# Kernel optimization log

Measured on AMD Instinct MI355X. Metric: run time of the kernel, lower is better.

Reference implementation:

```python
import jax, jax.numpy as jnp
import numpy as np

MAX_IT = 10
LAMBDA_ROF = 4.0
SIGMA = 1.0 / (7.0 * 0.01)
TAU = 0.01
THETA = 0.5
M, N = 2048, 2048


def forward_grad(x):
    """x: [1,M,N] -> [2,M,N]; forward differences, zero at last col/row."""
    gh = jnp.pad(x[0, :, 1:] - x[0, :, :-1], ((0, 0), (0, 1)))  # horizontal
    gv = jnp.pad(x[0, 1:, :] - x[0, :-1, :], ((0, 1), (0, 0)))  # vertical
    return jnp.stack([gh, gv], axis=0)


def backward_div(y):
    """y: [2,M,N] -> [1,M,N]; adjoint backward-difference divergence."""
    yh, yv = y[0], y[1]
    d_h = jnp.concatenate([yh[:, :1], yh[:, 1:-1] - yh[:, :-2], -yh[:, -2:-1]], axis=1)
    d_v = jnp.concatenate([yv[:1, :], yv[1:-1, :] - yv[:-2, :], -yv[-2:-1, :]], axis=0)
    return (d_h + d_v)[None]  # [1,M,N]


def prox_linf_ball(p, r):
    # Torch original builds m1/m2 from p.data (no grad flow) -> stop_gradient.
    m1 = jnp.maximum(p - r, 0.0)
    m2 = jnp.maximum(-p - r, 0.0)
    return p - jax.lax.stop_gradient(m1 - m2)  # == clamp(p, -r, r) in value


def setup_inputs() -> dict:
    key = jax.random.key(0)
    k1, k2 = jax.random.split(key)
    img_obs = jax.random.uniform(k1, (1, M, N), dtype=jnp.float32)
    w1 = jnp.array([0.5], dtype=jnp.float32)  # nn.Parameter [1]
    w2 = jnp.array([0.4], dtype=jnp.float32)  # nn.Parameter [1]
    return {"img_obs": img_obs, "w1": w1, "w2": w2}


def reference(img_obs, w1, w2):
    x = img_obs
    x_tilde = img_obs
    y = forward_grad(x)  # [2,M,N]
    # w_term built from y.data in torch -> constant wrt autodiff
    w_term = jax.lax.stop_gradient(jnp.exp(-jnp.abs(y)))
    w = w1[0] + w2[0] * w_term  # [2,M,N]
    for _ in range(MAX_IT):
        # dual weighted update + L-inf prox
        y = y + SIGMA * w * forward_grad(x_tilde)
        y = prox_linf_ball(y, 1.0)
        # primal weighted update (ROF)
        x_old = x
        x = (x + TAU * backward_div(w * y) + LAMBDA_ROF * TAU * img_obs) / (1.0 + LAMBDA_ROF * TAU)
        # primal over-relaxation
        x_tilde = x + THETA * (x - x_old)
    return x_tilde
```

## Files before the change

kernel.cpp:

```cpp
#include <hip/hip_runtime.h>


namespace {
constexpr int M = 2048, N = 2048;
constexpr float SIGMA     = 1.0f / (7.0f * 0.01f);
constexpr float TAU       = 0.01f;
constexpr float TAUIS     = TAU * (7.0f * 0.01f);
constexpr float LT        = 4.0f * 0.01f;
constexpr float INV_DEN   = 1.0f / (1.0f + 4.0f * 0.01f);
constexpr int TW = 64, TH = 64;
constexpr int PC = 88;
constexpr int PR = 84;
constexpr int UPR = 22;
constexpr int PROC = 83;
constexpr int NU = PROC * UPR;
constexpr int NT = 1024;
constexpr int NPASS = 2;
}

typedef _Float16 h4 __attribute__((ext_vector_type(4)));

__device__ inline h4 h4splat(float v) {
    _Float16 s = (_Float16)v;
    return (h4){s, s, s, s};
}
__device__ inline int imax(int a, int b) { return a > b ? a : b; }

__global__ __launch_bounds__(NT, 4) void pd_fused(
    const float* __restrict__ img, float* __restrict__ out,
    const float* __restrict__ w1p, const float* __restrict__ w2p)
{
    __shared__ __align__(16) float    sXT[PR * PC];
    __shared__ __align__(16) _Float16 sQH[PR * PC];
    __shared__ __align__(16) _Float16 sQV[PR * PC];

    const int tid  = threadIdx.x;
    const int lane = tid & 63;
    const int c0 = blockIdx.x * TW, r0 = blockIdx.y * TH;
    const int gr0 = r0 - 10, gc0 = c0 - 12;
    const float w1 = w1p[0], w2 = w2p[0];

    int u_[NPASS], bF_[NPASS], gi_[NPASS], gjb_[NPASS], dth_[NPASS];
    #pragma unroll
    for (int p = 0; p < NPASS; ++p) {
        int u = tid + p * NT;
        int li = u / UPR, uj = u - li * UPR;
        int lc = uj * 4;
        u_[p] = u; bF_[p] = u * 4;
        gi_[p] = gr0 + li; gjb_[p] = gc0 + lc;
        int d = imax(imax(9 - li, li - 73), imax(8 - lc, lc - 75));
        d = imax(d, 0);
        if (u >= NU) d = 100;
        dth_[p] = d;
    }

    #pragma unroll
    for (int p = 0; p < NPASS; ++p) {
        int su = tid + p * NT;
        if (su < PR * UPR) {
            int li = su / UPR, uj = su - li * UPR;
            int gi = gr0 + li, gj = gc0 + uj * 4;
            float4 v = make_float4(0.f, 0.f, 0.f, 0.f);
            if ((unsigned)gi < (unsigned)M && (unsigned)gj <= (unsigned)(N - 4))
                v = *(const float4*)&img[(size_t)gi * N + gj];
            *(float4*)&sXT[su * 4] = v;
        }
    }
    __syncthreads();

    float xr[NPASS][4], xi[NPASS][4], xt[NPASS][4];
    h4 yh[NPASS], yv[NPASS], swh[NPASS], swv[NPASS], qH[NPASS], qV[NPASS];

    #pragma unroll
    for (int p = 0; p < NPASS; ++p) {
        int u = u_[p], bF = bF_[p];
        float4 c = make_float4(0.f, 0.f, 0.f, 0.f);
        if (u < NU) c = *(const float4*)&sXT[bF];
        float rr = __shfl_down(c.x, 1, 64);
        if (u < NU) {
            if (lane == 63) rr = sXT[bF + 4];
            float4 dn = *(const float4*)&sXT[bF + PC];
            float ca[4] = {c.x, c.y, c.z, c.w};
            float da[4] = {dn.x, dn.y, dn.z, dn.w};
            int gi = gi_[p];
            bool rok = (unsigned)gi < (unsigned)M;
            bool vok = rok && (gi < M - 1);
            #pragma unroll
            for (int l = 0; l < 4; ++l) {
                int gj = gjb_[p] + l;
                bool cok = (unsigned)gj < (unsigned)N;
                bool hok = rok && cok && (gj < N - 1);
                bool vk  = vok && cok;
                float nxt = (l < 3) ? ca[l + 1] : rr;
                float gh = hok ? nxt - ca[l] : 0.f;
                float gv = vk  ? da[l] - ca[l] : 0.f;
                float wh = fmaf(w2, __expf(-fabsf(gh)), w1);
                float wv = fmaf(w2, __expf(-fabsf(gv)), w1);
                float y0h = fminf(fmaxf(gh * fmaf(SIGMA, wh, 1.f), -1.f), 1.f);
                float y0v = fminf(fmaxf(gv * fmaf(SIGMA, wv, 1.f), -1.f), 1.f);
                float sh = hok ? SIGMA * wh : 0.f;
                float sv = vk  ? SIGMA * wv : 0.f;
                yh[p][l]  = (_Float16)y0h;  yv[p][l]  = (_Float16)y0v;
                swh[p][l] = (_Float16)sh;   swv[p][l] = (_Float16)sv;
                qH[p][l]  = (_Float16)(sh * y0h);
                qV[p][l]  = (_Float16)(sv * y0v);
                xr[p][l] = ca[l]; xi[p][l] = ca[l]; xt[p][l] = ca[l];
            }
            *(h4*)&sQH[bF] = qH[p]; *(h4*)&sQV[bF] = qV[p];
        }
    }
    __syncthreads();

    auto dual = [&](int rem) {
        #pragma unroll
        for (int p = 0; p < NPASS; ++p) {
            float rr = __shfl_down(xt[p][0], 1, 64);
            if (rem >= dth_[p]) {
                int bF = bF_[p];
                if (lane == 63) rr = sXT[bF + 4];
                float4 dn = *(const float4*)&sXT[bF + PC];
                float da[4] = {dn.x, dn.y, dn.z, dn.w};
                h4 ghh, gvh;
                #pragma unroll
                for (int l = 0; l < 4; ++l) {
                    float nxt = (l < 3) ? xt[p][l + 1] : rr;
                    ghh[l] = (_Float16)(nxt - xt[p][l]);
                    gvh[l] = (_Float16)(da[l] - xt[p][l]);
                }
                h4 nh = yh[p] + swh[p] * ghh;
                h4 nv = yv[p] + swv[p] * gvh;
                nh = __builtin_elementwise_min(__builtin_elementwise_max(nh, h4splat(-1.f)), h4splat(1.f));
                nv = __builtin_elementwise_min(__builtin_elementwise_max(nv, h4splat(-1.f)), h4splat(1.f));
                yh[p] = nh; yv[p] = nv;
                h4 qh = swh[p] * nh;
                h4 qv = swv[p] * nv;
                qH[p] = qh; qV[p] = qv;
                *(h4*)&sQH[bF] = qh; *(h4*)&sQV[bF] = qv;
            }
        }
    };

    auto primal = [&](int rem) {
        #pragma unroll
        for (int p = 0; p < NPASS; ++p) {
            if (rem >= dth_[p]) {
                int u = u_[p], bF = bF_[p];
                int bu = (u >= UPR) ? bF - PC : bF;
                h4 qvu = *(const h4*)&sQV[bu];
                _Float16 qhl = sQH[imax(bF - 1, 0)];
                h4 qsh;
                qsh[0] = qhl; qsh[1] = qH[p][0]; qsh[2] = qH[p][1]; qsh[3] = qH[p][2];
                h4 dvg = (qH[p] - qsh) + (qV[p] - qvu);
                float xtv[4];
                #pragma unroll
                for (int l = 0; l < 4; ++l) {
                    float dv = (float)dvg[l];
                    float xo = xr[p][l];
                    float xn = (fmaf(TAUIS, dv, xo) + LT * xi[p][l]) * INV_DEN;
                    xr[p][l] = xn;
                    float v = fmaf(0.5f, xn - xo, xn);
                    xt[p][l] = v; xtv[l] = v;
                }
                *(float4*)&sXT[bF] = make_float4(xtv[0], xtv[1], xtv[2], xtv[3]);
            }
        }
    };

    primal(9);
    __syncthreads();
    #pragma unroll 1
    for (int t = 1; t < 10; ++t) {
        int rem = 9 - t;
        dual(rem);
        __syncthreads();
        primal(rem);
        __syncthreads();
    }

    {
        int row = tid >> 4;
        int cu  = tid & 15;
        float4 v = *(const float4*)&sXT[(10 + row) * PC + 12 + 4 * cu];
        *(float4*)&out[(size_t)(r0 + row) * N + (c0 + 4 * cu)] = v;
    }
}

extern "C" void kernel_launch(void* const* d_in, const int* in_sizes, int n_in,
                              void* d_out, int out_size, void* d_ws, size_t ws_size,
                              hipStream_t stream)
{
    const float* img = (const float*)d_in[0];
    const float* w1  = (const float*)d_in[1];
    const float* w2  = (const float*)d_in[2];
    float* out = (float*)d_out;

    dim3 grid(N / TW, M / TH);
    pd_fused<<<grid, NT, 0, stream>>>(img, out, w1, w2);
}
```

Baseline: 120.2 us.

## Shrink tiles to 64x48 with 512 threads and trim shared/register state

Reduces the tile height to 48 rows and the block to 512 threads, with three work units per thread, and adds a ragged-edge guard on the output store. To cut register and LDS pressure, the full sQH array is replaced by a small array that holds only the last horizontal-flux element of each unit, qV is reloaded from LDS instead of kept in registers, and the observed image copy is stored as fp16. The goal is more resident blocks per CU. The cost is a larger halo overhead relative to the tile (68 rows loaded for 48 output rows), a partial last block row, and extra fp16 rounding in the fidelity term.

```diff
diff --git a/kernel.cpp b/kernel.cpp
--- a/kernel.cpp
+++ b/kernel.cpp
@@ -8,14 +8,15 @@
 constexpr float TAUIS     = TAU * (7.0f * 0.01f);
 constexpr float LT        = 4.0f * 0.01f;
 constexpr float INV_DEN   = 1.0f / (1.0f + 4.0f * 0.01f);
-constexpr int TW = 64, TH = 64;
+constexpr int TW = 64, TH = 48;
 constexpr int PC = 88;
-constexpr int PR = 84;
+constexpr int PR = 68;
 constexpr int UPR = 22;
-constexpr int PROC = 83;
+constexpr int PROC = 67;
 constexpr int NU = PROC * UPR;
-constexpr int NT = 1024;
-constexpr int NPASS = 2;
+constexpr int NT = 512;
+constexpr int NPASS = 3;
+constexpr int GY = (M + TH - 1) / TH;
 }
 
 typedef _Float16 h4 __attribute__((ext_vector_type(4)));
@@ -31,8 +32,8 @@
     const float* __restrict__ w1p, const float* __restrict__ w2p)
 {
     __shared__ __align__(16) float    sXT[PR * PC];
-    __shared__ __align__(16) _Float16 sQH[PR * PC];
     __shared__ __align__(16) _Float16 sQV[PR * PC];
+    __shared__ __align__(16) _Float16 sQH3[1536];
 
     const int tid  = threadIdx.x;
     const int lane = tid & 63;
@@ -40,15 +41,14 @@
     const int gr0 = r0 - 10, gc0 = c0 - 12;
     const float w1 = w1p[0], w2 = w2p[0];
 
-    int u_[NPASS], bF_[NPASS], gi_[NPASS], gjb_[NPASS], dth_[NPASS];
+    int bF_[NPASS], dth_[NPASS];
     #pragma unroll
     for (int p = 0; p < NPASS; ++p) {
         int u = tid + p * NT;
         int li = u / UPR, uj = u - li * UPR;
         int lc = uj * 4;
-        u_[p] = u; bF_[p] = u * 4;
-        gi_[p] = gr0 + li; gjb_[p] = gc0 + lc;
-        int d = imax(imax(9 - li, li - 73), imax(8 - lc, lc - 75));
+        bF_[p] = u * 4;
+        int d = imax(imax(9 - li, li - (TH + 9)), imax(8 - lc, lc - 75));
         d = imax(d, 0);
         if (u >= NU) d = 100;
         dth_[p] = d;
@@ -68,26 +68,28 @@
     }
     __syncthreads();
 
-    float xr[NPASS][4], xi[NPASS][4], xt[NPASS][4];
-    h4 yh[NPASS], yv[NPASS], swh[NPASS], swv[NPASS], qH[NPASS], qV[NPASS];
+    float xr[NPASS][4], xt[NPASS][4];
+    h4 xi[NPASS], yh[NPASS], yv[NPASS], swh[NPASS], swv[NPASS], qH[NPASS];
 
     #pragma unroll
     for (int p = 0; p < NPASS; ++p) {
-        int u = u_[p], bF = bF_[p];
+        int u = tid + p * NT, bF = bF_[p];
         float4 c = make_float4(0.f, 0.f, 0.f, 0.f);
         if (u < NU) c = *(const float4*)&sXT[bF];
         float rr = __shfl_down(c.x, 1, 64);
         if (u < NU) {
+            int li = u / UPR;
+            int gi = gr0 + li, gjb = gc0 + (u - li * UPR) * 4;
             if (lane == 63) rr = sXT[bF + 4];
             float4 dn = *(const float4*)&sXT[bF + PC];
             float ca[4] = {c.x, c.y, c.z, c.w};
             float da[4] = {dn.x, dn.y, dn.z, dn.w};
-            int gi = gi_[p];
             bool rok = (unsigned)gi < (unsigned)M;
             bool vok = rok && (gi < M - 1);
+            h4 qv;
             #pragma unroll
             for (int l = 0; l < 4; ++l) {
-                int gj = gjb_[p] + l;
+                int gj = gjb + l;
                 bool cok = (unsigned)gj < (unsigned)N;
                 bool hok = rok && cok && (gj < N - 1);
                 bool vk  = vok && cok;
@@ -103,10 +105,12 @@
                 yh[p][l]  = (_Float16)y0h;  yv[p][l]  = (_Float16)y0v;
                 swh[p][l] = (_Float16)sh;   swv[p][l] = (_Float16)sv;
                 qH[p][l]  = (_Float16)(sh * y0h);
-                qV[p][l]  = (_Float16)(sv * y0v);
-                xr[p][l] = ca[l]; xi[p][l] = ca[l]; xt[p][l] = ca[l];
+                qv[l]     = (_Float16)(sv * y0v);
+                xr[p][l] = ca[l]; xt[p][l] = ca[l];
+                xi[p][l] = (_Float16)ca[l];
             }
-            *(h4*)&sQH[bF] = qH[p]; *(h4*)&sQV[bF] = qV[p];
+            *(h4*)&sQV[bF] = qv;
+            sQH3[u] = qH[p][3];
         }
     }
     __syncthreads();
@@ -134,8 +138,9 @@
                 yh[p] = nh; yv[p] = nv;
                 h4 qh = swh[p] * nh;
                 h4 qv = swv[p] * nv;
-                qH[p] = qh; qV[p] = qv;
-                *(h4*)&sQH[bF] = qh; *(h4*)&sQV[bF] = qv;
+                qH[p] = qh;
+                *(h4*)&sQV[bF] = qv;
+                sQH3[bF >> 2] = qh[3];
             }
         }
     };
@@ -144,19 +149,20 @@
         #pragma unroll
         for (int p = 0; p < NPASS; ++p) {
             if (rem >= dth_[p]) {
-                int u = u_[p], bF = bF_[p];
-                int bu = (u >= UPR) ? bF - PC : bF;
+                int bF = bF_[p];
+                int bu = (bF >= UPR * 4) ? bF - PC : bF;
                 h4 qvu = *(const h4*)&sQV[bu];
-                _Float16 qhl = sQH[imax(bF - 1, 0)];
+                h4 qv  = *(const h4*)&sQV[bF];
+                _Float16 qhl = sQH3[imax((bF >> 2) - 1, 0)];
                 h4 qsh;
                 qsh[0] = qhl; qsh[1] = qH[p][0]; qsh[2] = qH[p][1]; qsh[3] = qH[p][2];
-                h4 dvg = (qH[p] - qsh) + (qV[p] - qvu);
+                h4 dvg = (qH[p] - qsh) + (qv - qvu);
                 float xtv[4];
                 #pragma unroll
                 for (int l = 0; l < 4; ++l) {
                     float dv = (float)dvg[l];
                     float xo = xr[p][l];
-                    float xn = (fmaf(TAUIS, dv, xo) + LT * xi[p][l]) * INV_DEN;
+                    float xn = (fmaf(TAUIS, dv, xo) + LT * (float)xi[p][l]) * INV_DEN;
                     xr[p][l] = xn;
                     float v = fmaf(0.5f, xn - xo, xn);
                     xt[p][l] = v; xtv[l] = v;
@@ -177,11 +183,15 @@
         __syncthreads();
     }
 
-    {
-        int row = tid >> 4;
-        int cu  = tid & 15;
-        float4 v = *(const float4*)&sXT[(10 + row) * PC + 12 + 4 * cu];
-        *(float4*)&out[(size_t)(r0 + row) * N + (c0 + 4 * cu)] = v;
+    #pragma unroll
+    for (int v = tid; v < TH * (TW / 4); v += NT) {
+        int row = v >> 4;
+        int cu  = v & 15;
+        int gi = r0 + row;
+        if (gi < M) {
+            float4 o = *(const float4*)&sXT[(10 + row) * PC + 12 + 4 * cu];
+            *(float4*)&out[(size_t)gi * N + (c0 + 4 * cu)] = o;
+        }
     }
 }
 
@@ -194,6 +204,6 @@
     const float* w2  = (const float*)d_in[2];
     float* out = (float*)d_out;
 
-    dim3 grid(N / TW, M / TH);
+    dim3 grid(N / TW, GY);
     pd_fused<<<grid, NT, 0, stream>>>(img, out, w1, w2);
 }
```

After: 121.9 us. Within noise of the previous version (+1.4%).
